# Kernel optimization log

Measured on AMD Instinct MI355X. Metric: run time of the kernel, lower is better.

## Reference

```python
import jax, jax.numpy as jnp
import numpy as np

# Canonical Mamba hyperparams (mamba_ssm defaults for d_model=128)
D_MODEL = 128
D_INNER = 2 * D_MODEL          # expand = 2
D_STATE = 16
D_CONV = 4
DT_RANK = (D_MODEL + 15) // 16  # ceil(d_model/16) = 8
B, N, T = 16, 256, 64
EPS = 1e-5


def setup_inputs() -> dict:
    key = jax.random.key(0)
    ks = jax.random.split(key, 10)
    sc = 0.02
    x = jax.random.normal(ks[0], (B, N, D_MODEL, T), jnp.float32)
    gamma = jnp.ones((D_MODEL,), jnp.float32)
    beta = jnp.zeros((D_MODEL,), jnp.float32)
    W_in = jax.random.normal(ks[1], (D_MODEL, 2 * D_INNER), jnp.float32) * sc
    conv_w = jax.random.normal(ks[2], (D_INNER, D_CONV), jnp.float32) * sc
    conv_b = jnp.zeros((D_INNER,), jnp.float32)
    W_x = jax.random.normal(ks[3], (D_INNER, DT_RANK + 2 * D_STATE), jnp.float32) * sc
    W_dt = jax.random.normal(ks[4], (DT_RANK, D_INNER), jnp.float32) * sc
    b_dt = jax.random.normal(ks[5], (D_INNER,), jnp.float32) * sc
    # S4D-real init: A_log = log(1..d_state), broadcast over channels
    A_log = jnp.log(jnp.broadcast_to(
        jnp.arange(1, D_STATE + 1, dtype=jnp.float32), (D_INNER, D_STATE)))
    Dskip = jnp.ones((D_INNER,), jnp.float32)
    W_out = jax.random.normal(ks[6], (D_INNER, D_MODEL), jnp.float32) * sc
    return dict(x=x, gamma=gamma, beta=beta, W_in=W_in, conv_w=conv_w,
                conv_b=conv_b, W_x=W_x, W_dt=W_dt, b_dt=b_dt,
                A_log=A_log, Dskip=Dskip, W_out=W_out)


def _forward(x, gamma, beta, W_in, conv_w, conv_b, W_x, W_dt, b_dt,
             A_log, Dskip, W_out):
    Bb, Nn, Fd, Tt = x.shape
    # (B,N,F,T) -> (B*N, T, F)
    x_in = x.transpose(0, 1, 3, 2).reshape(Bb * Nn, Tt, Fd)

    # LayerNorm over feature dim
    mu = x_in.mean(-1, keepdims=True)
    var = jnp.mean((x_in - mu) ** 2, axis=-1, keepdims=True)
    u = (x_in - mu) * jax.lax.rsqrt(var + EPS) * gamma + beta

    # Mamba: input projection -> (x, z)
    xz = u @ W_in                                   # (BN,T,2*dI)
    xc, z = jnp.split(xz, 2, axis=-1)

    # Depthwise causal conv1d over time (kernel D_CONV) + SiLU
    xp = jnp.pad(xc, ((0, 0), (D_CONV - 1, 0), (0, 0)))
    xconv = sum(xp[:, k:k + Tt, :] * conv_w[:, k] for k in range(D_CONV)) + conv_b
    xact = jax.nn.silu(xconv)                       # (BN,T,dI)

    # Input-dependent SSM parameters
    dbl = xact @ W_x                                # (BN,T,dt_rank+2*dS)
    dt = dbl[..., :DT_RANK]
    Bm = dbl[..., DT_RANK:DT_RANK + D_STATE]        # (BN,T,dS)
    Cm = dbl[..., DT_RANK + D_STATE:]               # (BN,T,dS)
    delta = jax.nn.softplus(dt @ W_dt + b_dt)       # (BN,T,dI)
    A = -jnp.exp(A_log)                             # (dI,dS)

    # Selective scan over time
    def step(h, inp):
        d, b, c, xt = inp                            # (BN,dI) (BN,dS) (BN,dS) (BN,dI)
        dA = jnp.exp(d[:, :, None] * A)              # (BN,dI,dS)
        h = dA * h + (d * xt)[:, :, None] * b[:, None, :]
        y = jnp.einsum('bis,bs->bi', h, c)
        return h, y

    h0 = jnp.zeros((Bb * Nn, D_INNER, D_STATE), x.dtype)
    seq = (delta.transpose(1, 0, 2), Bm.transpose(1, 0, 2),
           Cm.transpose(1, 0, 2), xact.transpose(1, 0, 2))
    _, ys = jax.lax.scan(step, h0, seq)             # (T,BN,dI)
    y = ys.transpose(1, 0, 2) + xact * Dskip
    y = y * jax.nn.silu(z)
    out = y @ W_out                                 # (BN,T,d_model)

    # Residual (dropout is identity in eval/reference), reshape back
    x_out = out + x_in
    return x_out.reshape(Bb, Nn, Tt, Fd).transpose(0, 1, 3, 2)


def reference(x, gamma, beta, W_in, conv_w, conv_b, W_x, W_dt, b_dt,
              A_log, Dskip, W_out):
    return _forward(x, gamma, beta, W_in, conv_w, conv_b, W_x, W_dt, b_dt,
                    A_log, Dskip, W_out)
```

## Files before the change

### kernel.cpp

```cpp
#include <hip/hip_runtime.h>
#include <stdint.h>

typedef unsigned short ushort_t;
typedef __attribute__((ext_vector_type(8))) short bf16x8;
typedef __attribute__((ext_vector_type(4))) float f32x4;
typedef __attribute__((ext_vector_type(2))) float f32x2;

#define P_CONVW 0
#define P_CONVB 1024
#define P_BDT   1280
#define P_A     1536
#define P_DSKIP 5632
#define P_GAMMA 5888
#define P_BETA  6016
#define P_WDT   6144
#define P_TOT   8192

#define OFFB_WINT   0
#define OFFB_WXT    131072
#define OFFB_WOUTT  163840
#define OFFB_PF     229376
#define OFFB_DYN    262144

__device__ __forceinline__ float b2f(ushort_t u) {
    return __uint_as_float(((unsigned int)u) << 16);
}
__device__ __forceinline__ ushort_t f2b(float f) {
    unsigned int x = __float_as_uint(f);
    return (ushort_t)((x + 0x7fffu + ((x >> 16) & 1u)) >> 16);
}
__device__ __forceinline__ bool is_f32_mode(const void* gamma) {
    return ((const unsigned int*)gamma)[0] == 0x3F800000u;
}
__device__ __forceinline__ float ld_any(const void* p, int idx, bool f32m) {
    return f32m ? ((const float*)p)[idx] : b2f(((const ushort_t*)p)[idx]);
}
__device__ __forceinline__ float silu_f(float v) {
    return v * __builtin_amdgcn_rcpf(1.0f + __expf(-v));
}
__device__ __forceinline__ f32x2 pk_fma(f32x2 a, f32x2 b, f32x2 c) {
    f32x2 d; asm("v_pk_fma_f32 %0, %1, %2, %3" : "=v"(d) : "v"(a), "v"(b), "v"(c)); return d;
}
__device__ __forceinline__ f32x2 pk_mul(f32x2 a, f32x2 b) {
    f32x2 d; asm("v_pk_mul_f32 %0, %1, %2" : "=v"(d) : "v"(a), "v"(b)); return d;
}
__device__ __forceinline__ f32x2 pk_add(f32x2 a, f32x2 b) {
    f32x2 d; asm("v_pk_add_f32 %0, %1, %2" : "=v"(d) : "v"(a), "v"(b)); return d;
}

__global__ __launch_bounds__(256) void prep_kernel(
    const void* __restrict__ gamma, const void* __restrict__ beta,
    const void* __restrict__ W_in,  const void* __restrict__ conv_w,
    const void* __restrict__ conv_b,const void* __restrict__ W_x,
    const void* __restrict__ W_dt,  const void* __restrict__ b_dt,
    const void* __restrict__ A_log, const void* __restrict__ Dskip,
    const void* __restrict__ W_out, char* __restrict__ wsb)
{
    const bool f32m = is_f32_mode(gamma);
    ushort_t* WinT  = (ushort_t*)(wsb + OFFB_WINT);
    ushort_t* WxT   = (ushort_t*)(wsb + OFFB_WXT);
    ushort_t* WoutT = (ushort_t*)(wsb + OFFB_WOUTT);
    float*    pf    = (float*)(wsb + OFFB_PF);
    int idx = blockIdx.x * 256 + threadIdx.x;

    if (idx < 65536) {
        int n = idx >> 7, k = idx & 127;
        WinT[idx] = f2b(ld_any(W_in, k * 512 + n, f32m));
    }
    if (idx < 16384) {
        int n = idx >> 8, k = idx & 255;
        WxT[idx] = (n < 40) ? f2b(ld_any(W_x, k * 40 + n, f32m)) : (ushort_t)0;
    }
    if (idx < 32768) {
        int n = idx >> 8, k = idx & 255;
        WoutT[idx] = f2b(ld_any(W_out, k * 128 + n, f32m));
    }
    if (idx < 1024) pf[P_CONVW + idx] = ld_any(conv_w, idx, f32m);
    if (idx < 4096) pf[P_A + idx]     = -__expf(ld_any(A_log, idx, f32m));
    if (idx < 2048) pf[P_WDT + idx]   = ld_any(W_dt, idx, f32m);
    if (idx < 256) {
        pf[P_CONVB + idx] = ld_any(conv_b, idx, f32m);
        pf[P_BDT + idx]   = ld_any(b_dt, idx, f32m);
        pf[P_DSKIP + idx] = ld_any(Dskip, idx, f32m);
    }
    if (idx < 128) {
        pf[P_GAMMA + idx] = ld_any(gamma, idx, f32m);
        pf[P_BETA + idx]  = ld_any(beta, idx, f32m);
    }
}

__global__ __launch_bounds__(256, 3) void k_mamba(
    const void* __restrict__ x_v, const void* __restrict__ gamma_v,
    const float* __restrict__ pf, const ushort_t* __restrict__ WinT,
    const ushort_t* __restrict__ WxT, const ushort_t* __restrict__ WoutT,
    ushort_t* __restrict__ xz, void* __restrict__ out_v, int seq_base)
{
    __shared__ __align__(16) char smem[51712];
    float*    uT     = (float*)smem;
    ushort_t* xact_s = (ushort_t*)smem;
    ushort_t* Afr    = (ushort_t*)(smem + 34816);
    float*    red1   = (float*)(smem + 34816);
    float*    red2   = (float*)(smem + 34816 + 1024);
    float*    dt_s   = (float*)(smem + 34816);
    ushort_t* BC_s   = (ushort_t*)(smem + 36864);
    float*    mu_s   = (float*)(smem + 51200);
    float*    rs_s   = (float*)(smem + 51456);

    const int tid = threadIdx.x;
    const int sloc = blockIdx.x;
    const int sglob = seq_base + sloc;
    const bool f32m = is_f32_mode(gamma_v);
    const int lane = tid & 63, w = tid >> 6;
    const int r = lane & 15, q = lane >> 4;
    const size_t seq_off = (size_t)sglob * 8192;
    const size_t xzbase = (size_t)sloc * 32768;

    {
        int f = tid >> 1, th = tid & 1;
        float* dst = uT + f * 68 + th * 32;
        if (!f32m) {
            const uint4* src = (const uint4*)((const ushort_t*)x_v + seq_off + f * 64 + th * 32);
            #pragma unroll
            for (int i = 0; i < 4; ++i) {
                uint4 qd = src[i];
                *(float4*)(dst + i * 8) = make_float4(
                    __uint_as_float(qd.x << 16), __uint_as_float(qd.x & 0xffff0000u),
                    __uint_as_float(qd.y << 16), __uint_as_float(qd.y & 0xffff0000u));
                *(float4*)(dst + i * 8 + 4) = make_float4(
                    __uint_as_float(qd.z << 16), __uint_as_float(qd.z & 0xffff0000u),
                    __uint_as_float(qd.w << 16), __uint_as_float(qd.w & 0xffff0000u));
            }
        } else {
            const float4* src = (const float4*)((const float*)x_v + seq_off + f * 64 + th * 32);
            #pragma unroll
            for (int i = 0; i < 8; ++i) *(float4*)(dst + i * 4) = src[i];
        }
    }
    __syncthreads();

    {
        int qq = tid >> 6, t = tid & 63;
        float su = 0.f, sq = 0.f;
        #pragma unroll 8
        for (int kk = 0; kk < 32; ++kk) {
            float v = uT[(qq * 32 + kk) * 68 + t];
            su += v; sq += v * v;
        }
        red1[tid] = su; red2[tid] = sq;
    }
    __syncthreads();
    if (tid < 64) {
        float su = red1[tid] + red1[64 + tid] + red1[128 + tid] + red1[192 + tid];
        float sq = red2[tid] + red2[64 + tid] + red2[128 + tid] + red2[192 + tid];
        float mu = su * (1.0f / 128.0f);
        float var = sq * (1.0f / 128.0f) - mu * mu;
        mu_s[tid] = mu;
        rs_s[tid] = rsqrtf(var + 1e-5f);
    }
    __syncthreads();

    {
        int t = tid & 63, dq = tid >> 6;
        float mu = mu_s[t], rs = rs_s[t];
        int mf = t >> 4, rr = t & 15;
        #pragma unroll
        for (int k = 0; k < 4; ++k) {
            unsigned int pk4[4];
            #pragma unroll
            for (int e = 0; e < 4; ++e) {
                int d0 = dq * 32 + k * 8 + 2 * e;
                float v0 = (uT[d0 * 68 + t] - mu) * rs * pf[P_GAMMA + d0] + pf[P_BETA + d0];
                float v1 = (uT[(d0 + 1) * 68 + t] - mu) * rs * pf[P_GAMMA + d0 + 1] + pf[P_BETA + d0 + 1];
                pk4[e] = (unsigned int)f2b(v0) | ((unsigned int)f2b(v1) << 16);
            }
            *(uint4*)(Afr + ((dq * 4 + mf) * 64 + k * 16 + rr) * 8) =
                make_uint4(pk4[0], pk4[1], pk4[2], pk4[3]);
        }
    }
    __syncthreads();

    {
        #pragma unroll 1
        for (int nh = 0; nh < 2; ++nh) {
            f32x4 acc[4][4];
            #pragma unroll
            for (int i = 0; i < 4; ++i)
                #pragma unroll
                for (int nf = 0; nf < 4; ++nf) acc[i][nf] = (f32x4)(0.0f);

            #pragma unroll
            for (int ks = 0; ks < 4; ++ks) {
                bf16x8 a[4], b[4];
                #pragma unroll
                for (int i = 0; i < 4; ++i)
                    a[i] = *(const bf16x8*)(Afr + ((ks * 4 + i) * 64 + lane) * 8);
                #pragma unroll
                for (int nf = 0; nf < 4; ++nf) {
                    int n = w * 128 + nh * 64 + nf * 16 + r;
                    b[nf] = *(const bf16x8*)(WinT + (size_t)n * 128 + ks * 32 + q * 8);
                }
                #pragma unroll
                for (int i = 0; i < 4; ++i)
                    #pragma unroll
                    for (int nf = 0; nf < 4; ++nf)
                        acc[i][nf] = __builtin_amdgcn_mfma_f32_16x16x32_bf16(a[i], b[nf], acc[i][nf], 0, 0, 0);
            }
            #pragma unroll
            for (int i = 0; i < 4; ++i)
                #pragma unroll
                for (int nf = 0; nf < 4; ++nf) {
                    int n = w * 128 + nh * 64 + nf * 16 + r;
                    int tb = i * 16 + q * 4;
                    uint2 res;
                    res.x = (unsigned int)f2b(acc[i][nf][0]) |
                            ((unsigned int)f2b(acc[i][nf][1]) << 16);
                    res.y = (unsigned int)f2b(acc[i][nf][2]) |
                            ((unsigned int)f2b(acc[i][nf][3]) << 16);
                    *(uint2*)(xz + xzbase + (size_t)n * 64 + tb) = res;
                }
        }
    }
    __syncthreads();

    {
        const int c = tid;
        float cw0 = pf[P_CONVW + c * 4 + 0], cw1 = pf[P_CONVW + c * 4 + 1];
        float cw2 = pf[P_CONVW + c * 4 + 2], cw3 = pf[P_CONVW + c * 4 + 3];
        float cb  = pf[P_CONVB + c];
        float w0 = 0.f, w1 = 0.f, w2 = 0.f;
        const uint4* xq = (const uint4*)(xz + xzbase + (size_t)c * 64);
        #pragma unroll
        for (int ch = 0; ch < 4; ++ch) {
            uint4 a0 = xq[2 * ch], a1 = xq[2 * ch + 1];
            unsigned int wds[8] = {a0.x, a0.y, a0.z, a0.w, a1.x, a1.y, a1.z, a1.w};
            #pragma unroll
            for (int jj = 0; jj < 8; ++jj) {
                unsigned int v = wds[jj];
                int t = ch * 16 + jj * 2;
                float xv0 = __uint_as_float(v << 16);
                float o0 = cb + w0 * cw0 + w1 * cw1 + w2 * cw2 + xv0 * cw3;
                xact_s[t * 264 + c] = f2b(silu_f(o0));
                w0 = w1; w1 = w2; w2 = xv0;
                float xv1 = __uint_as_float(v & 0xffff0000u);
                float o1 = cb + w0 * cw0 + w1 * cw1 + w2 * cw2 + xv1 * cw3;
                xact_s[(t + 1) * 264 + c] = f2b(silu_f(o1));
                w0 = w1; w1 = w2; w2 = xv1;
            }
        }
    }
    __syncthreads();

    {
        f32x4 acc2[4];
        #pragma unroll
        for (int i = 0; i < 4; ++i) acc2[i] = (f32x4)(0.0f);
        #pragma unroll 1
        for (int ks = 0; ks < 8; ++ks) {
            bf16x8 b = *(const bf16x8*)(WxT + (w * 16 + r) * 256 + ks * 32 + q * 8);
            #pragma unroll
            for (int i = 0; i < 4; ++i) {
                bf16x8 a = *(const bf16x8*)(xact_s + (i * 16 + r) * 264 + ks * 32 + q * 8);
                acc2[i] = __builtin_amdgcn_mfma_f32_16x16x32_bf16(a, b, acc2[i], 0, 0, 0);
            }
        }
        int col = w * 16 + r;
        #pragma unroll
        for (int i = 0; i < 4; ++i)
            #pragma unroll
            for (int rg = 0; rg < 4; ++rg) {
                int trow = i * 16 + q * 4 + rg;
                float v = acc2[i][rg];
                if (col < 8)       dt_s[trow * 8 + col] = v;
                else if (col < 40) BC_s[trow * 40 + (col - 8)] = f2b(v);
            }
    }
    __syncthreads();

    {
        const int i = tid;
        float wdt[8];
        #pragma unroll
        for (int rr = 0; rr < 8; ++rr) wdt[rr] = pf[P_WDT + rr * 256 + i];
        const float bdt = pf[P_BDT + i];
        const float dsk = pf[P_DSKIP + i];

        bool structured = true;
        #pragma unroll
        for (int ss = 0; ss < 16; ++ss) {
            float av = pf[P_A + i * 16 + ss];
            structured = structured && (fabsf(av + (float)(ss + 1)) <= 1e-3f * (float)(ss + 1));
        }

        const ushort_t* zrow = xz + xzbase + (size_t)(256 + i) * 64;

        auto dt_arg = [&](int t) -> float {
            const float* dr = dt_s + t * 8;
            float4 d0 = *(const float4*)dr;
            float4 d1 = *(const float4*)(dr + 4);
            float arg = bdt;
            arg = fmaf(d0.x, wdt[0], arg); arg = fmaf(d0.y, wdt[1], arg);
            arg = fmaf(d0.z, wdt[2], arg); arg = fmaf(d0.w, wdt[3], arg);
            arg = fmaf(d1.x, wdt[4], arg); arg = fmaf(d1.y, wdt[5], arg);
            arg = fmaf(d1.z, wdt[6], arg); arg = fmaf(d1.w, wdt[7], arg);
            return arg;
        };

        if (structured) {
            f32x2 h2[8];
            #pragma unroll
            for (int p = 0; p < 8; ++p) h2[p] = (f32x2){0.f, 0.f};

            f32x2 dAA[8], dAB[8];
            float dxA, xtA, sgA, dxB, xtB, sgB;

            auto PF = [&](int t, f32x2* dA, float& dx, float& xt, float& sg, ushort_t zv) {
                float arg = dt_arg(t);
                float p = __expf(arg);
                float opp = 1.0f + p;
                float e1 = __builtin_amdgcn_rcpf(opp);
                float del = __logf(opp);
                float e2 = e1 * e1, e4 = e2 * e2, e8 = e4 * e4;
                f32x2 m2 = {e2, e2}, m4 = {e4, e4}, m8 = {e8, e8};
                dA[0] = (f32x2){e1, e2};
                dA[1] = pk_mul(dA[0], m2);
                dA[2] = pk_mul(dA[0], m4);
                dA[3] = pk_mul(dA[1], m4);
                dA[4] = pk_mul(dA[0], m8);
                dA[5] = pk_mul(dA[1], m8);
                dA[6] = pk_mul(dA[2], m8);
                dA[7] = pk_mul(dA[3], m8);
                xt = b2f(xact_s[t * 264 + i]);
                dx = del * xt;
                sg = silu_f(b2f(zv));
            };

            auto STEP = [&](int t, const f32x2* dA, float dx, float xt, float sg) -> float {
                const uint4* bq = (const uint4*)(BC_s + t * 40);
                uint4 b0 = bq[0], b1 = bq[1], b2v = bq[2], b3 = bq[3];
                unsigned int pw[16] = {b0.x, b0.y, b0.z, b0.w, b1.x, b1.y, b1.z, b1.w,
                                       b2v.x, b2v.y, b2v.z, b2v.w, b3.x, b3.y, b3.z, b3.w};
                f32x2 dx2 = {dx, dx};
                f32x2 ya = {0.f, 0.f}, yb = {0.f, 0.f};
                #pragma unroll
                for (int p = 0; p < 8; ++p) {
                    unsigned int v = pw[p];
                    f32x2 B2 = {__uint_as_float(v << 16), __uint_as_float(v & 0xffff0000u)};
                    unsigned int vc = pw[8 + p];
                    f32x2 C2 = {__uint_as_float(vc << 16), __uint_as_float(vc & 0xffff0000u)};
                    f32x2 bx = pk_mul(B2, dx2);
                    h2[p] = pk_fma(dA[p], h2[p], bx);
                    if (p & 1) yb = pk_fma(h2[p], C2, yb);
                    else       ya = pk_fma(h2[p], C2, ya);
                }
                f32x2 ys = pk_add(ya, yb);
                float y = ys[0] + ys[1];
                return fmaf(xt, dsk, y) * sg;
            };

            const unsigned int* zr = (const unsigned int*)zrow;
            unsigned int zw_c = zr[0];
            PF(0, dAA, dxA, xtA, sgA, (ushort_t)(zw_c & 0xffffu));

            #pragma unroll 1
            for (int t = 0; t < 64; t += 2) {
                int wn = (t >> 1) + 1; if (wn > 31) wn = 31;
                unsigned int zw_n = zr[wn];
                PF(t + 1, dAB, dxB, xtB, sgB, (ushort_t)(zw_c >> 16));
                float ygA = STEP(t, dAA, dxA, xtA, sgA);
                int t2 = (t + 2 > 63) ? 63 : t + 2;
                PF(t2, dAA, dxA, xtA, sgA, (ushort_t)(zw_n & 0xffffu));
                float ygB = STEP(t + 1, dAB, dxB, xtB, sgB);
                unsigned int pkk;
                asm("v_cvt_pk_bf16_f32 %0, %1, %2" : "=v"(pkk) : "v"(ygA), "v"(ygB));
                xact_s[t * 264 + i] = (ushort_t)(pkk & 0xffffu);
                xact_s[(t + 1) * 264 + i] = (ushort_t)(pkk >> 16);
                zw_c = zw_n;
            }
        } else {
            float Av[16];
            #pragma unroll
            for (int ss = 0; ss < 16; ++ss) Av[ss] = pf[P_A + i * 16 + ss];
            float h[16];
            #pragma unroll
            for (int ss = 0; ss < 16; ++ss) h[ss] = 0.f;
            #pragma unroll 1
            for (int t = 0; t < 64; ++t) {
                float arg = dt_arg(t);
                float delta = __logf(1.0f + __expf(arg));
                unsigned int pk[16];
                const uint2* bq = (const uint2*)(BC_s + t * 40);
                #pragma unroll
                for (int jj = 0; jj < 8; ++jj) {
                    uint2 vv = bq[jj];
                    pk[2 * jj] = vv.x; pk[2 * jj + 1] = vv.y;
                }
                float Bv[16], Cv[16];
                #pragma unroll
                for (int jj = 0; jj < 8; ++jj) {
                    unsigned int v = pk[jj];
                    Bv[2 * jj]     = __uint_as_float(v << 16);
                    Bv[2 * jj + 1] = __uint_as_float(v & 0xffff0000u);
                    unsigned int vc = pk[8 + jj];
                    Cv[2 * jj]     = __uint_as_float(vc << 16);
                    Cv[2 * jj + 1] = __uint_as_float(vc & 0xffff0000u);
                }
                float xt = b2f(xact_s[t * 264 + i]);
                float zf = b2f(zrow[t]);
                float dx = delta * xt;
                float y = 0.f;
                #pragma unroll
                for (int ss = 0; ss < 16; ++ss) {
                    float dA = __expf(delta * Av[ss]);
                    h[ss] = fmaf(dA, h[ss], dx * Bv[ss]);
                    y = fmaf(h[ss], Cv[ss], y);
                }
                float yg = fmaf(xt, dsk, y) * silu_f(zf);
                xact_s[t * 264 + i] = f2b(yg);
            }
        }
    }
    __syncthreads();

    {
        f32x4 acc3[4][2];
        #pragma unroll
        for (int i = 0; i < 4; ++i)
            #pragma unroll
            for (int nf = 0; nf < 2; ++nf) acc3[i][nf] = (f32x4)(0.0f);
        #pragma unroll 1
        for (int ks = 0; ks < 8; ++ks) {
            bf16x8 a[4], b[2];
            #pragma unroll
            for (int i = 0; i < 4; ++i)
                a[i] = *(const bf16x8*)(xact_s + (i * 16 + r) * 264 + ks * 32 + q * 8);
            #pragma unroll
            for (int nf = 0; nf < 2; ++nf)
                b[nf] = *(const bf16x8*)(WoutT + (w * 32 + nf * 16 + r) * 256 + ks * 32 + q * 8);
            #pragma unroll
            for (int i = 0; i < 4; ++i)
                #pragma unroll
                for (int nf = 0; nf < 2; ++nf)
                    acc3[i][nf] = __builtin_amdgcn_mfma_f32_16x16x32_bf16(a[i], b[nf], acc3[i][nf], 0, 0, 0);
        }
        if (!f32m) {
            #pragma unroll
            for (int i = 0; i < 4; ++i)
                #pragma unroll
                for (int nf = 0; nf < 2; ++nf) {
                    int d = w * 32 + nf * 16 + r;
                    int tb = i * 16 + q * 4;
                    size_t off = seq_off + (size_t)d * 64 + tb;
                    uint2 xv = *(const uint2*)((const ushort_t*)x_v + off);
                    float x0 = __uint_as_float(xv.x << 16);
                    float x1 = __uint_as_float(xv.x & 0xffff0000u);
                    float x2 = __uint_as_float(xv.y << 16);
                    float x3 = __uint_as_float(xv.y & 0xffff0000u);
                    uint2 res;
                    res.x = (unsigned int)f2b(acc3[i][nf][0] + x0) |
                            ((unsigned int)f2b(acc3[i][nf][1] + x1) << 16);
                    res.y = (unsigned int)f2b(acc3[i][nf][2] + x2) |
                            ((unsigned int)f2b(acc3[i][nf][3] + x3) << 16);
                    *(uint2*)((ushort_t*)out_v + off) = res;
                }
        } else {
            #pragma unroll
            for (int i = 0; i < 4; ++i)
                #pragma unroll
                for (int nf = 0; nf < 2; ++nf) {
                    int d = w * 32 + nf * 16 + r;
                    int tb = i * 16 + q * 4;
                    size_t off = seq_off + (size_t)d * 64 + tb;
                    float4 xv = *(const float4*)((const float*)x_v + off);
                    float4 res = make_float4(acc3[i][nf][0] + xv.x,
                                             acc3[i][nf][1] + xv.y,
                                             acc3[i][nf][2] + xv.z,
                                             acc3[i][nf][3] + xv.w);
                    *(float4*)((float*)out_v + off) = res;
                }
        }
    }
}

extern "C" void kernel_launch(void* const* d_in, const int* in_sizes, int n_in,
                              void* d_out, int out_size, void* d_ws, size_t ws_size,
                              hipStream_t stream)
{
    const void* x      = d_in[0];
    const void* gamma  = d_in[1];
    const void* beta   = d_in[2];
    const void* W_in   = d_in[3];
    const void* conv_w = d_in[4];
    const void* conv_b = d_in[5];
    const void* W_x    = d_in[6];
    const void* W_dt   = d_in[7];
    const void* b_dt   = d_in[8];
    const void* A_log  = d_in[9];
    const void* Dskip  = d_in[10];
    const void* W_out  = d_in[11];

    char* wsb = (char*)d_ws;
    long long avail = (long long)ws_size - OFFB_DYN;
    long long S = avail > 0 ? avail / 65536 : 1;
    if (S > 4096) S = 4096;
    if (S < 1) S = 1;

    ushort_t* WinT  = (ushort_t*)(wsb + OFFB_WINT);
    ushort_t* WxT   = (ushort_t*)(wsb + OFFB_WXT);
    ushort_t* WoutT = (ushort_t*)(wsb + OFFB_WOUTT);
    float*    pf    = (float*)(wsb + OFFB_PF);
    ushort_t* xz_buf= (ushort_t*)(wsb + OFFB_DYN);

    prep_kernel<<<dim3(256), dim3(256), 0, stream>>>(
        gamma, beta, W_in, conv_w, conv_b, W_x, W_dt, b_dt, A_log, Dskip, W_out, wsb);

    for (int base = 0; base < 4096; base += (int)S) {
        int cnt = 4096 - base < (int)S ? 4096 - base : (int)S;
        k_mamba<<<dim3(cnt), dim3(256), 0, stream>>>(
            x, gamma, pf, WinT, WxT, WoutT, xz_buf, d_out, base);
    }
}
```

Before: 666.4 us.

## Keep xz projection in LDS instead of global scratch, precompute silu(z)

```diff
diff --git a/kernel.cpp b/kernel.cpp
--- a/kernel.cpp
+++ b/kernel.cpp
@@ -14,13 +14,21 @@
 #define P_GAMMA 5888
 #define P_BETA  6016
 #define P_WDT   6144
-#define P_TOT   8192
 
 #define OFFB_WINT   0
 #define OFFB_WXT    131072
 #define OFFB_WOUTT  163840
 #define OFFB_PF     229376
-#define OFFB_DYN    262144
+
+#define L_AFR   34816
+#define L_SG    34816
+#define L_RED1  68608
+#define L_RED2  69632
+#define L_MU    70656
+#define L_RS    70912
+#define L_DT    68608
+#define L_BC    70656
+#define LDS_TOTAL 78848
 
 __device__ __forceinline__ float b2f(ushort_t u) {
     return __uint_as_float(((unsigned int)u) << 16);
@@ -89,31 +97,31 @@
     }
 }
 
-__global__ __launch_bounds__(256, 3) void k_mamba(
+__global__ __launch_bounds__(256, 2) void k_mamba(
     const void* __restrict__ x_v, const void* __restrict__ gamma_v,
     const float* __restrict__ pf, const ushort_t* __restrict__ WinT,
     const ushort_t* __restrict__ WxT, const ushort_t* __restrict__ WoutT,
-    ushort_t* __restrict__ xz, void* __restrict__ out_v, int seq_base)
+    void* __restrict__ out_v)
 {
-    __shared__ __align__(16) char smem[51712];
+    extern __shared__ __align__(16) char smem[];
     float*    uT     = (float*)smem;
+    ushort_t* xc_s   = (ushort_t*)smem;
     ushort_t* xact_s = (ushort_t*)smem;
-    ushort_t* Afr    = (ushort_t*)(smem + 34816);
-    float*    red1   = (float*)(smem + 34816);
-    float*    red2   = (float*)(smem + 34816 + 1024);
-    float*    dt_s   = (float*)(smem + 34816);
-    ushort_t* BC_s   = (ushort_t*)(smem + 36864);
-    float*    mu_s   = (float*)(smem + 51200);
-    float*    rs_s   = (float*)(smem + 51456);
+    ushort_t* Afr    = (ushort_t*)(smem + L_AFR);
+    ushort_t* sg_s   = (ushort_t*)(smem + L_SG);
+    float*    red1   = (float*)(smem + L_RED1);
+    float*    red2   = (float*)(smem + L_RED2);
+    float*    mu_s   = (float*)(smem + L_MU);
+    float*    rs_s   = (float*)(smem + L_RS);
+    float*    dt_s   = (float*)(smem + L_DT);
+    float*    BC_s   = (float*)(smem + L_BC);
 
     const int tid = threadIdx.x;
-    const int sloc = blockIdx.x;
-    const int sglob = seq_base + sloc;
+    const int sglob = blockIdx.x;
     const bool f32m = is_f32_mode(gamma_v);
     const int lane = tid & 63, w = tid >> 6;
     const int r = lane & 15, q = lane >> 4;
     const size_t seq_off = (size_t)sglob * 8192;
-    const size_t xzbase = (size_t)sloc * 32768;
 
     {
         int f = tid >> 1, th = tid & 1;
@@ -180,45 +188,91 @@
     __syncthreads();
 
     {
-        #pragma unroll 1
-        for (int nh = 0; nh < 2; ++nh) {
-            f32x4 acc[4][4];
-            #pragma unroll
-            for (int i = 0; i < 4; ++i)
-                #pragma unroll
-                for (int nf = 0; nf < 4; ++nf) acc[i][nf] = (f32x4)(0.0f);
-
-            #pragma unroll
-            for (int ks = 0; ks < 4; ++ks) {
-                bf16x8 a[4], b[4];
-                #pragma unroll
-                for (int i = 0; i < 4; ++i)
-                    a[i] = *(const bf16x8*)(Afr + ((ks * 4 + i) * 64 + lane) * 8);
-                #pragma unroll
-                for (int nf = 0; nf < 4; ++nf) {
-                    int n = w * 128 + nh * 64 + nf * 16 + r;
-                    b[nf] = *(const bf16x8*)(WinT + (size_t)n * 128 + ks * 32 + q * 8);
-                }
-                #pragma unroll
-                for (int i = 0; i < 4; ++i)
-                    #pragma unroll
-                    for (int nf = 0; nf < 4; ++nf)
-                        acc[i][nf] = __builtin_amdgcn_mfma_f32_16x16x32_bf16(a[i], b[nf], acc[i][nf], 0, 0, 0);
-            }
-            #pragma unroll
-            for (int i = 0; i < 4; ++i)
-                #pragma unroll
-                for (int nf = 0; nf < 4; ++nf) {
-                    int n = w * 128 + nh * 64 + nf * 16 + r;
-                    int tb = i * 16 + q * 4;
-                    uint2 res;
-                    res.x = (unsigned int)f2b(acc[i][nf][0]) |
-                            ((unsigned int)f2b(acc[i][nf][1]) << 16);
-                    res.y = (unsigned int)f2b(acc[i][nf][2]) |
-                            ((unsigned int)f2b(acc[i][nf][3]) << 16);
-                    *(uint2*)(xz + xzbase + (size_t)n * 64 + tb) = res;
-                }
-        }
+        f32x4 acc[4][4];
+        #pragma unroll
+        for (int i = 0; i < 4; ++i)
+            #pragma unroll
+            for (int nf = 0; nf < 4; ++nf) acc[i][nf] = (f32x4)(0.0f);
+        #pragma unroll
+        for (int ks = 0; ks < 4; ++ks) {
+            bf16x8 a[4], b[4];
+            #pragma unroll
+            for (int i = 0; i < 4; ++i)
+                a[i] = *(const bf16x8*)(Afr + ((ks * 4 + i) * 64 + lane) * 8);
+            #pragma unroll
+            for (int nf = 0; nf < 4; ++nf) {
+                int n = w * 64 + nf * 16 + r;
+                b[nf] = *(const bf16x8*)(WinT + (size_t)n * 128 + ks * 32 + q * 8);
+            }
+            #pragma unroll
+            for (int i = 0; i < 4; ++i)
+                #pragma unroll
+                for (int nf = 0; nf < 4; ++nf)
+                    acc[i][nf] = __builtin_amdgcn_mfma_f32_16x16x32_bf16(a[i], b[nf], acc[i][nf], 0, 0, 0);
+        }
+        #pragma unroll
+        for (int i = 0; i < 4; ++i)
+            #pragma unroll
+            for (int nf = 0; nf < 4; ++nf) {
+                int n = w * 64 + nf * 16 + r;
+                int tb = i * 16 + q * 4;
+                unsigned int p01 = (unsigned int)f2b(acc[i][nf][0]) |
+                                   ((unsigned int)f2b(acc[i][nf][1]) << 16);
+                unsigned int p23 = (unsigned int)f2b(acc[i][nf][2]) |
+                                   ((unsigned int)f2b(acc[i][nf][3]) << 16);
+                ushort_t* dst = xc_s + n * 66 + tb;
+                *(unsigned int*)(dst)     = p01;
+                *(unsigned int*)(dst + 2) = p23;
+            }
+    }
+
+    {
+        f32x4 acc[4][4];
+        #pragma unroll
+        for (int i = 0; i < 4; ++i)
+            #pragma unroll
+            for (int nf = 0; nf < 4; ++nf) acc[i][nf] = (f32x4)(0.0f);
+        #pragma unroll
+        for (int ks = 0; ks < 4; ++ks) {
+            bf16x8 a[4], b[4];
+            #pragma unroll
+            for (int i = 0; i < 4; ++i)
+                a[i] = *(const bf16x8*)(Afr + ((ks * 4 + i) * 64 + lane) * 8);
+            #pragma unroll
+            for (int nf = 0; nf < 4; ++nf) {
+                int n = 256 + w * 64 + nf * 16 + r;
+                b[nf] = *(const bf16x8*)(WinT + (size_t)n * 128 + ks * 32 + q * 8);
+            }
+            #pragma unroll
+            for (int i = 0; i < 4; ++i)
+                #pragma unroll
+                for (int nf = 0; nf < 4; ++nf)
+                    acc[i][nf] = __builtin_amdgcn_mfma_f32_16x16x32_bf16(a[i], b[nf], acc[i][nf], 0, 0, 0);
+        }
+        __syncthreads();
+        #pragma unroll
+        for (int i = 0; i < 4; ++i)
+            #pragma unroll
+            for (int nf = 0; nf < 4; ++nf) {
+                int cz = w * 64 + nf * 16 + r;
+                int tb = i * 16 + q * 4;
+                float s0 = silu_f(acc[i][nf][0]);
+                float s1 = silu_f(acc[i][nf][1]);
+                float s2 = silu_f(acc[i][nf][2]);
+                float s3 = silu_f(acc[i][nf][3]);
+                unsigned int p01 = (unsigned int)f2b(s0) | ((unsigned int)f2b(s1) << 16);
+                unsigned int p23 = (unsigned int)f2b(s2) | ((unsigned int)f2b(s3) << 16);
+                ushort_t* dst = sg_s + cz * 66 + tb;
+                *(unsigned int*)(dst)     = p01;
+                *(unsigned int*)(dst + 2) = p23;
+            }
+    }
+
+    unsigned int cpk[32];
+    {
+        const unsigned int* row = (const unsigned int*)(xc_s + tid * 66);
+        #pragma unroll
+        for (int j = 0; j < 32; ++j) cpk[j] = row[j];
     }
     __syncthreads();
 
@@ -228,24 +282,18 @@
         float cw2 = pf[P_CONVW + c * 4 + 2], cw3 = pf[P_CONVW + c * 4 + 3];
         float cb  = pf[P_CONVB + c];
         float w0 = 0.f, w1 = 0.f, w2 = 0.f;
-        const uint4* xq = (const uint4*)(xz + xzbase + (size_t)c * 64);
-        #pragma unroll
-        for (int ch = 0; ch < 4; ++ch) {
-            uint4 a0 = xq[2 * ch], a1 = xq[2 * ch + 1];
-            unsigned int wds[8] = {a0.x, a0.y, a0.z, a0.w, a1.x, a1.y, a1.z, a1.w};
-            #pragma unroll
-            for (int jj = 0; jj < 8; ++jj) {
-                unsigned int v = wds[jj];
-                int t = ch * 16 + jj * 2;
-                float xv0 = __uint_as_float(v << 16);
-                float o0 = cb + w0 * cw0 + w1 * cw1 + w2 * cw2 + xv0 * cw3;
-                xact_s[t * 264 + c] = f2b(silu_f(o0));
-                w0 = w1; w1 = w2; w2 = xv0;
-                float xv1 = __uint_as_float(v & 0xffff0000u);
-                float o1 = cb + w0 * cw0 + w1 * cw1 + w2 * cw2 + xv1 * cw3;
-                xact_s[(t + 1) * 264 + c] = f2b(silu_f(o1));
-                w0 = w1; w1 = w2; w2 = xv1;
-            }
+        #pragma unroll
+        for (int j = 0; j < 32; ++j) {
+            unsigned int v = cpk[j];
+            int t = 2 * j;
+            float xv0 = __uint_as_float(v << 16);
+            float o0 = cb + w0 * cw0 + w1 * cw1 + w2 * cw2 + xv0 * cw3;
+            xact_s[t * 264 + c] = f2b(silu_f(o0));
+            w0 = w1; w1 = w2; w2 = xv0;
+            float xv1 = __uint_as_float(v & 0xffff0000u);
+            float o1 = cb + w0 * cw0 + w1 * cw1 + w2 * cw2 + xv1 * cw3;
+            xact_s[(t + 1) * 264 + c] = f2b(silu_f(o1));
+            w0 = w1; w1 = w2; w2 = xv1;
         }
     }
     __syncthreads();
@@ -271,7 +319,7 @@
                 int trow = i * 16 + q * 4 + rg;
                 float v = acc2[i][rg];
                 if (col < 8)       dt_s[trow * 8 + col] = v;
-                else if (col < 40) BC_s[trow * 40 + (col - 8)] = f2b(v);
+                else if (col < 40) BC_s[trow * 32 + (col - 8)] = v;
             }
     }
     __syncthreads();
@@ -290,8 +338,6 @@
             float av = pf[P_A + i * 16 + ss];
             structured = structured && (fabsf(av + (float)(ss + 1)) <= 1e-3f * (float)(ss + 1));
         }
-
-        const ushort_t* zrow = xz + xzbase + (size_t)(256 + i) * 64;
 
         auto dt_arg = [&](int t) -> float {
             const float* dr = dt_s + t * 8;
@@ -313,7 +359,7 @@
             f32x2 dAA[8], dAB[8];
             float dxA, xtA, sgA, dxB, xtB, sgB;
 
-            auto PF = [&](int t, f32x2* dA, float& dx, float& xt, float& sg, ushort_t zv) {
+            auto PF = [&](int t, f32x2* dA, float& dx, float& xt, float& sg) {
                 float arg = dt_arg(t);
                 float p = __expf(arg);
                 float opp = 1.0f + p;
@@ -331,50 +377,43 @@
                 dA[7] = pk_mul(dA[3], m8);
                 xt = b2f(xact_s[t * 264 + i]);
                 dx = del * xt;
-                sg = silu_f(b2f(zv));
+                sg = b2f(sg_s[i * 66 + t]);
             };
 
             auto STEP = [&](int t, const f32x2* dA, float dx, float xt, float sg) -> float {
-                const uint4* bq = (const uint4*)(BC_s + t * 40);
-                uint4 b0 = bq[0], b1 = bq[1], b2v = bq[2], b3 = bq[3];
-                unsigned int pw[16] = {b0.x, b0.y, b0.z, b0.w, b1.x, b1.y, b1.z, b1.w,
-                                       b2v.x, b2v.y, b2v.z, b2v.w, b3.x, b3.y, b3.z, b3.w};
+                const f32x4* br = (const f32x4*)(BC_s + t * 32);
+                f32x4 b0 = br[0], b1 = br[1], b2v = br[2], b3 = br[3];
+                f32x4 c0 = br[4], c1 = br[5], c2v = br[6], c3 = br[7];
+                f32x2 Bp[8] = {{b0[0],b0[1]},{b0[2],b0[3]},{b1[0],b1[1]},{b1[2],b1[3]},
+                               {b2v[0],b2v[1]},{b2v[2],b2v[3]},{b3[0],b3[1]},{b3[2],b3[3]}};
+                f32x2 Cp[8] = {{c0[0],c0[1]},{c0[2],c0[3]},{c1[0],c1[1]},{c1[2],c1[3]},
+                               {c2v[0],c2v[1]},{c2v[2],c2v[3]},{c3[0],c3[1]},{c3[2],c3[3]}};
                 f32x2 dx2 = {dx, dx};
                 f32x2 ya = {0.f, 0.f}, yb = {0.f, 0.f};
                 #pragma unroll
                 for (int p = 0; p < 8; ++p) {
-                    unsigned int v = pw[p];
-                    f32x2 B2 = {__uint_as_float(v << 16), __uint_as_float(v & 0xffff0000u)};
-                    unsigned int vc = pw[8 + p];
-                    f32x2 C2 = {__uint_as_float(vc << 16), __uint_as_float(vc & 0xffff0000u)};
-                    f32x2 bx = pk_mul(B2, dx2);
+                    f32x2 bx = pk_mul(Bp[p], dx2);
                     h2[p] = pk_fma(dA[p], h2[p], bx);
-                    if (p & 1) yb = pk_fma(h2[p], C2, yb);
-                    else       ya = pk_fma(h2[p], C2, ya);
+                    if (p & 1) yb = pk_fma(h2[p], Cp[p], yb);
+                    else       ya = pk_fma(h2[p], Cp[p], ya);
                 }
                 f32x2 ys = pk_add(ya, yb);
                 float y = ys[0] + ys[1];
                 return fmaf(xt, dsk, y) * sg;
             };
 
-            const unsigned int* zr = (const unsigned int*)zrow;
-            unsigned int zw_c = zr[0];
-            PF(0, dAA, dxA, xtA, sgA, (ushort_t)(zw_c & 0xffffu));
-
+            PF(0, dAA, dxA, xtA, sgA);
             #pragma unroll 1
             for (int t = 0; t < 64; t += 2) {
-                int wn = (t >> 1) + 1; if (wn > 31) wn = 31;
-                unsigned int zw_n = zr[wn];
-                PF(t + 1, dAB, dxB, xtB, sgB, (ushort_t)(zw_c >> 16));
+                PF(t + 1, dAB, dxB, xtB, sgB);
                 float ygA = STEP(t, dAA, dxA, xtA, sgA);
                 int t2 = (t + 2 > 63) ? 63 : t + 2;
-                PF(t2, dAA, dxA, xtA, sgA, (ushort_t)(zw_n & 0xffffu));
+                PF(t2, dAA, dxA, xtA, sgA);
                 float ygB = STEP(t + 1, dAB, dxB, xtB, sgB);
                 unsigned int pkk;
                 asm("v_cvt_pk_bf16_f32 %0, %1, %2" : "=v"(pkk) : "v"(ygA), "v"(ygB));
                 xact_s[t * 264 + i] = (ushort_t)(pkk & 0xffffu);
                 xact_s[(t + 1) * 264 + i] = (ushort_t)(pkk >> 16);
-                zw_c = zw_n;
             }
         } else {
             float Av[16];
@@ -387,34 +426,18 @@
             for (int t = 0; t < 64; ++t) {
                 float arg = dt_arg(t);
                 float delta = __logf(1.0f + __expf(arg));
-                unsigned int pk[16];
-                const uint2* bq = (const uint2*)(BC_s + t * 40);
-                #pragma unroll
-                for (int jj = 0; jj < 8; ++jj) {
-                    uint2 vv = bq[jj];
-                    pk[2 * jj] = vv.x; pk[2 * jj + 1] = vv.y;
-                }
-                float Bv[16], Cv[16];
-                #pragma unroll
-                for (int jj = 0; jj < 8; ++jj) {
-                    unsigned int v = pk[jj];
-                    Bv[2 * jj]     = __uint_as_float(v << 16);
-                    Bv[2 * jj + 1] = __uint_as_float(v & 0xffff0000u);
-                    unsigned int vc = pk[8 + jj];
-                    Cv[2 * jj]     = __uint_as_float(vc << 16);
-                    Cv[2 * jj + 1] = __uint_as_float(vc & 0xffff0000u);
-                }
+                const float* brow = BC_s + t * 32;
                 float xt = b2f(xact_s[t * 264 + i]);
-                float zf = b2f(zrow[t]);
+                float sgv = b2f(sg_s[i * 66 + t]);
                 float dx = delta * xt;
                 float y = 0.f;
                 #pragma unroll
                 for (int ss = 0; ss < 16; ++ss) {
                     float dA = __expf(delta * Av[ss]);
-                    h[ss] = fmaf(dA, h[ss], dx * Bv[ss]);
-                    y = fmaf(h[ss], Cv[ss], y);
+                    h[ss] = fmaf(dA, h[ss], dx * brow[ss]);
+                    y = fmaf(h[ss], brow[16 + ss], y);
                 }
-                float yg = fmaf(xt, dsk, y) * silu_f(zf);
+                float yg = fmaf(xt, dsk, y) * sgv;
                 xact_s[t * 264 + i] = f2b(yg);
             }
         }
@@ -499,23 +522,22 @@
     const void* W_out  = d_in[11];
 
     char* wsb = (char*)d_ws;
-    long long avail = (long long)ws_size - OFFB_DYN;
-    long long S = avail > 0 ? avail / 65536 : 1;
-    if (S > 4096) S = 4096;
-    if (S < 1) S = 1;
-
     ushort_t* WinT  = (ushort_t*)(wsb + OFFB_WINT);
     ushort_t* WxT   = (ushort_t*)(wsb + OFFB_WXT);
     ushort_t* WoutT = (ushort_t*)(wsb + OFFB_WOUTT);
     float*    pf    = (float*)(wsb + OFFB_PF);
-    ushort_t* xz_buf= (ushort_t*)(wsb + OFFB_DYN);
+
+    static bool attr_set = false;
+    if (!attr_set) {
+        (void)hipFuncSetAttribute(reinterpret_cast<const void*>(k_mamba),
+                                  hipFuncAttributeMaxDynamicSharedMemorySize,
+                                  LDS_TOTAL);
+        attr_set = true;
+    }
 
     prep_kernel<<<dim3(256), dim3(256), 0, stream>>>(
         gamma, beta, W_in, conv_w, conv_b, W_x, W_dt, b_dt, A_log, Dskip, W_out, wsb);
 
-    for (int base = 0; base < 4096; base += (int)S) {
-        int cnt = 4096 - base < (int)S ? 4096 - base : (int)S;
-        k_mamba<<<dim3(cnt), dim3(256), 0, stream>>>(
-            x, gamma, pf, WinT, WxT, WoutT, xz_buf, d_out, base);
-    }
-}
+    k_mamba<<<dim3(4096), dim3(256), LDS_TOTAL, stream>>>(
+        x, gamma, pf, WinT, WxT, WoutT, d_out);
+}
```

After: 584.3 us. 12.3% less time.
